# Kernel optimization log

Hardware: AMD Instinct MI355X
Metric: run time of the kernel (lower is better)

## Reference

```python
import math
import jax, jax.numpy as jnp
import numpy as np

B, S, D = 2, 2048, 1024
H, DK = 16, 64
NUM_BUCKETS = 32
MAX_DISTANCE = 128


def _relative_position_bucket(relative_position, num_buckets=NUM_BUCKETS, max_distance=MAX_DISTANCE):
    # bidirectional=True branch (encoder / non-causal)
    n = -relative_position
    num_buckets = num_buckets // 2
    ret = (n < 0).astype(jnp.int32) * num_buckets
    n = jnp.abs(n)
    max_exact = num_buckets // 2
    is_small = n < max_exact
    # guard log(0); masked out by is_small anyway
    n_safe = jnp.maximum(n, 1).astype(jnp.float32)
    val_if_large = max_exact + (
        jnp.log(n_safe / max_exact) / math.log(max_distance / max_exact) * (num_buckets - max_exact)
    ).astype(jnp.int32)
    val_if_large = jnp.minimum(val_if_large, num_buckets - 1)
    return ret + jnp.where(is_small, n, val_if_large)


def setup_inputs() -> dict:
    key = jax.random.key(0)
    ks = jax.random.split(key, 6)
    std_q = (D * DK) ** -0.5
    std = D ** -0.5
    return {
        "x": jax.random.normal(ks[0], (B, S, D), jnp.float32),
        "q_w": jax.random.normal(ks[1], (H * DK, D), jnp.float32) * std_q,
        "k_w": jax.random.normal(ks[2], (H * DK, D), jnp.float32) * std,
        "v_w": jax.random.normal(ks[3], (H * DK, D), jnp.float32) * std,
        "o_w": jax.random.normal(ks[4], (D, H * DK), jnp.float32) * ((H * DK) ** -0.5),
        "rel_bias": jax.random.normal(ks[5], (NUM_BUCKETS, H), jnp.float32) * std,
    }


def reference(x, q_w, k_w, v_w, o_w, rel_bias):
    b, s, _ = x.shape
    # project and split heads: [B, H, S, DK]
    def proj(w):
        return (x @ w.T).reshape(b, s, H, DK).transpose(0, 2, 1, 3)
    q, k, v = proj(q_w), proj(k_w), proj(v_w)

    # T5-style unscaled attention scores: [B, H, Sq, Sk]
    scores = jnp.einsum("bhqd,bhkd->bhqk", q, k)

    # bucketed relative-position bias
    ctx = jnp.arange(s)[:, None]
    mem = jnp.arange(s)[None, :]
    rp_bucket = _relative_position_bucket(mem - ctx)  # [S, S]
    bias = rel_bias[rp_bucket]                        # [S, S, H]
    bias = bias.transpose(2, 0, 1)[None]              # [1, H, S, S]
    scores = scores + bias

    attn = jax.nn.softmax(scores, axis=-1)
    ctx_out = jnp.einsum("bhqk,bhkd->bhqd", attn, v)
    ctx_out = ctx_out.transpose(0, 2, 1, 3).reshape(b, s, H * DK)
    return ctx_out @ o_w.T
```

## Files before the change

### kernel.cpp

```cpp
#include <hip/hip_runtime.h>
#include <stdint.h>


typedef unsigned short u16;
typedef __attribute__((ext_vector_type(8))) short short8;
typedef __attribute__((ext_vector_type(4))) float float4v;
typedef __attribute__((ext_vector_type(4))) u16 ushort4v;
typedef __attribute__((ext_vector_type(4))) uint32_t uint4v;

typedef __attribute__((address_space(1))) void void_g;
typedef __attribute__((address_space(3))) void void_l;

#define L2E 1.4426950408889634f

__device__ __forceinline__ u16 f2b(float f) {
  union { float f; uint32_t u; } v; v.f = f;
  uint32_t r = (v.u + 0x7fffu + ((v.u >> 16) & 1u)) >> 16;
  return (u16)r;
}
__device__ __forceinline__ u16 f2b_fast(float f) {
  union { float f; uint32_t u; } v; v.f = f;
  return (u16)((v.u + 0x8000u) >> 16);
}

__global__ void cvt_all(const float* __restrict__ x,  const float* __restrict__ qw,
                        const float* __restrict__ kw, const float* __restrict__ vw,
                        const float* __restrict__ ow, const float* __restrict__ rel_bias,
                        u16* __restrict__ xb, u16* __restrict__ wqkv, u16* __restrict__ owb,
                        float* __restrict__ biasT) {
  int bi = blockIdx.x;
  if (bi >= 8192) {
    int idx = (bi - 8192) * 256 + threadIdx.x;
    int h = idx >> 12, t = idx & 4095;
    if (t > 4094) { biasT[h * 4096 + 4095] = -1.0e4f; return; }
    int d = t - 2047;
    int n = -d;
    int ret = (n < 0) ? 16 : 0;
    int na = (n < 0) ? -n : n;
    int bucket;
    if (na < 8) {
      bucket = ret + na;
    } else {
      float v = logf((float)na / 8.0f) / logf(16.0f) * 8.0f;
      int vi = 8 + (int)v;
      bucket = ret + (vi > 15 ? 15 : vi);
    }
    biasT[h * 4096 + t] = (rel_bias[bucket * 16 + h] - 8.0f) * L2E;
    return;
  }
  int i = bi * 256 + threadIdx.x;
  const float* s; u16* d; int off;
  if (i < 1048576)      { s = x;  d = xb;              off = i; }
  else if (i < 1310720) { s = qw; d = wqkv;            off = i - 1048576; }
  else if (i < 1572864) { s = kw; d = wqkv + 1048576;  off = i - 1310720; }
  else if (i < 1835008) { s = vw; d = wqkv + 2097152;  off = i - 1572864; }
  else                  { s = ow; d = owb;             off = i - 1835008; }
  float4v v = ((const float4v*)s)[off];
  ushort4v o;
  o.x = f2b(v.x); o.y = f2b(v.y); o.z = f2b(v.z); o.w = f2b(v.w);
  ((ushort4v*)d)[off] = o;
}

__global__ __launch_bounds__(256, 2)
void gemm_qkv(const u16* __restrict__ A, const u16* __restrict__ W,
              u16* __restrict__ qkb, u16* __restrict__ vTp) {
  const int K = 1024;
  __shared__ __align__(16) char SM[34816];
  u16* As = (u16*)SM;
  u16* Bs = (u16*)(SM + 16384);
  const int tid = threadIdx.x;
  const int wid = tid >> 6;
  const int lane = tid & 63;
  const int row16 = lane & 15, oct = lane >> 4;
  const int tm = blockIdx.x * 128, tn = blockIdx.y * 128;
  const int wm = (wid & 1) * 64, wn = (wid >> 1) * 64;
  const int srow = lane >> 2;
  const int sc = (lane & 3) * 8;
  float4v acc[4][4] = {};
  for (int k0 = 0; k0 < K; k0 += 64) {
    __syncthreads();
#pragma unroll
    for (int i = 0; i < 4; i++) {
      const int idx = i * 4 + wid;
      const int kk = idx & 1;
      const int rb = idx >> 1;
      const int r = rb * 16 + srow;
      const int c = kk * 32 + sc;
      __builtin_amdgcn_global_load_lds((void_g*)(A + (size_t)(tm + r) * K + k0 + c),
                                       (void_l*)(As + (kk * 128 + rb * 16) * 32), 16, 0, 0);
      __builtin_amdgcn_global_load_lds((void_g*)(W + (size_t)(tn + r) * K + k0 + c),
                                       (void_l*)(Bs + (kk * 128 + rb * 16) * 32), 16, 0, 0);
    }
    __syncthreads();
#pragma unroll
    for (int kk = 0; kk < 2; kk++) {
      short8 af[4], bfr[4];
#pragma unroll
      for (int mi = 0; mi < 4; mi++)
        af[mi] = *(const short8*)(As + (kk * 128 + wm + mi * 16 + row16) * 32 + oct * 8);
#pragma unroll
      for (int ni = 0; ni < 4; ni++)
        bfr[ni] = *(const short8*)(Bs + (kk * 128 + wn + ni * 16 + row16) * 32 + oct * 8);
#pragma unroll
      for (int mi = 0; mi < 4; mi++)
#pragma unroll
        for (int ni = 0; ni < 4; ni++)
          acc[mi][ni] = __builtin_amdgcn_mfma_f32_16x16x32_bf16(af[mi], bfr[ni], acc[mi][ni], 0, 0, 0);
    }
  }

  u16* Es = (u16*)SM;
  __syncthreads();
#pragma unroll
  for (int mi = 0; mi < 4; mi++)
#pragma unroll
    for (int ni = 0; ni < 4; ni++)
#pragma unroll
      for (int r = 0; r < 4; r++)
        Es[(wm + mi * 16 + oct * 4 + r) * 136 + wn + ni * 16 + row16] = f2b(acc[mi][ni][r]);
  __syncthreads();

  if (tn < 2048) {
#pragma unroll
    for (int it = 0; it < 8; it++) {
      int idx = it * 256 + tid;
      int row = idx >> 4, c = idx & 15;
      short8 v = *(const short8*)(Es + row * 136 + c * 8);
      *(short8*)(qkb + (size_t)(tm + row) * 2048 + tn + c * 8) = v;
    }
  } else {
    const int h0 = (tn - 2048) >> 6;
    const int b = tm >> 11;
    const int s0 = tm & 2047;
#pragma unroll
    for (int it = 0; it < 8; it++) {
      int idx = it * 256 + tid;
      int dg = idx >> 4;
      int ch = idx & 15;
      short8 o;
#pragma unroll
      for (int j = 0; j < 8; j++) {
        int sp = ch * 8 + j;
        int sl = (sp & ~31) + (((sp >> 2) & 1) << 4) + (((sp >> 3) & 3) << 2) + (sp & 3);
        o[j] = (short)Es[sl * 136 + dg];
      }
      const int head = h0 + (dg >> 6), d = dg & 63;
      *(short8*)(vTp + ((size_t)((b * 16 + head) * 64 + d)) * 2048 + s0 + ch * 8) = o;
    }
  }
}

__global__ __launch_bounds__(256, 2)
void gemm_out(const u16* __restrict__ A, const u16* __restrict__ W,
              float* __restrict__ C) {
  const int K = 1024, N = 1024;
  __shared__ __align__(16) char SM[34816];
  u16* As = (u16*)SM;
  u16* Bs = (u16*)(SM + 8192);
  const int tid = threadIdx.x;
  const int wid = tid >> 6;
  const int lane = tid & 63;
  const int row16 = lane & 15, oct = lane >> 4;
  const int tm = blockIdx.x * 64, tn = blockIdx.y * 128;
  const int wm = (wid & 1) * 32, wn = (wid >> 1) * 64;
  const int srow = lane >> 2;
  const int sc = (lane & 3) * 8;
  float4v acc[2][4] = {};
  for (int k0 = 0; k0 < K; k0 += 64) {
    __syncthreads();
#pragma unroll
    for (int i = 0; i < 2; i++) {
      const int idx = i * 4 + wid;
      const int kk = idx & 1;
      const int rb = idx >> 1;
      const int r = rb * 16 + srow;
      const int c = kk * 32 + sc;
      __builtin_amdgcn_global_load_lds((void_g*)(A + (size_t)(tm + r) * K + k0 + c),
                                       (void_l*)(As + (kk * 64 + rb * 16) * 32), 16, 0, 0);
    }
#pragma unroll
    for (int i = 0; i < 4; i++) {
      const int idx = i * 4 + wid;
      const int kk = idx & 1;
      const int rb = idx >> 1;
      const int r = rb * 16 + srow;
      const int c = kk * 32 + sc;
      __builtin_amdgcn_global_load_lds((void_g*)(W + (size_t)(tn + r) * K + k0 + c),
                                       (void_l*)(Bs + (kk * 128 + rb * 16) * 32), 16, 0, 0);
    }
    __syncthreads();
#pragma unroll
    for (int kk = 0; kk < 2; kk++) {
      short8 af[2], bfr[4];
#pragma unroll
      for (int mi = 0; mi < 2; mi++)
        af[mi] = *(const short8*)(As + (kk * 64 + wm + mi * 16 + row16) * 32 + oct * 8);
#pragma unroll
      for (int ni = 0; ni < 4; ni++)
        bfr[ni] = *(const short8*)(Bs + (kk * 128 + wn + ni * 16 + row16) * 32 + oct * 8);
#pragma unroll
      for (int mi = 0; mi < 2; mi++)
#pragma unroll
        for (int ni = 0; ni < 4; ni++)
          acc[mi][ni] = __builtin_amdgcn_mfma_f32_16x16x32_bf16(af[mi], bfr[ni], acc[mi][ni], 0, 0, 0);
    }
  }
  float* Ef = (float*)SM;
  __syncthreads();
#pragma unroll
  for (int mi = 0; mi < 2; mi++)
#pragma unroll
    for (int ni = 0; ni < 4; ni++)
#pragma unroll
      for (int r = 0; r < 4; r++)
        Ef[(wm + mi * 16 + oct * 4 + r) * 132 + wn + ni * 16 + row16] = acc[mi][ni][r];
  __syncthreads();
#pragma unroll
  for (int it = 0; it < 8; it++) {
    int idx = it * 256 + tid;
    int row = idx >> 5, c = idx & 31;
    float4v v = *(const float4v*)(Ef + row * 132 + c * 4);
    *(float4v*)(C + (size_t)(tm + row) * N + tn + c * 4) = v;
  }
}

__global__ __launch_bounds__(256, 2)
void flash_attn(const u16* __restrict__ qkb, const u16* __restrict__ vTp,
                const float* __restrict__ biasT, u16* __restrict__ ctx) {
  const int S = 2048, LDQ = 2048;
  const int lin = blockIdx.x + (blockIdx.y << 4) + (blockIdx.z << 8);
  const int V = (lin & 7) * 64 + (lin >> 3);
  const int qt0 = (V & 15) * 128;
  const int h = (V >> 4) & 15, b = V >> 8;
  const int tid = threadIdx.x, wid = tid >> 6, lane = tid & 63;
  const int row16 = lane & 15, oct = lane >> 4;

  __shared__ __align__(16) float biasS[2176];
  __shared__ __align__(16) u16 Ks[2][64][40];
  __shared__ __align__(16) u16 Vts[2][64][40];

  {
    const float* bsrc = biasT + h * 4096 + (1920 - qt0);
    for (int i = tid; i < 544; i += 256)
      ((float4v*)biasS)[i] = ((const float4v*)bsrc)[i];
  }
  const float bias_neg = biasT[h * 4096];
  const float bias_pos = biasT[h * 4096 + 4094];

  const u16* qbase = qkb + ((size_t)b * S + qt0 + wid * 32) * LDQ + h * 64;
  short8 qf[2][2];
#pragma unroll
  for (int f = 0; f < 2; f++)
#pragma unroll
    for (int hd = 0; hd < 2; hd++)
      qf[f][hd] = *(const short8*)(qbase + (size_t)(f * 16 + row16) * LDQ + hd * 32 + oct * 8);

  float4v l_acc[2] = {};
  float4v o_acc[2][4] = {};
  const short8 ones = {0x3F80, 0x3F80, 0x3F80, 0x3F80, 0x3F80, 0x3F80, 0x3F80, 0x3F80};

  const int sr = lane >> 2, c8 = (lane & 3) * 8;
  const int srow = wid * 16 + sr;
  const u16* Kst = qkb + 1024 + ((size_t)b * S + srow) * LDQ + c8 + h * 64;
  const u16* Vst = vTp + ((size_t)(b * 16 + h) * 64 + srow) * 2048 + c8;

  short8 kreg[2], vreg[2];
#pragma unroll
  for (int hd = 0; hd < 2; hd++) kreg[hd] = *(const short8*)(Kst + hd * 32);
#pragma unroll
  for (int ks = 0; ks < 2; ks++) vreg[ks] = *(const short8*)(Vst + ks * 32);

  for (int kt = 0; kt < S; kt += 64) {
    __syncthreads();
#pragma unroll
    for (int hd = 0; hd < 2; hd++) *(short8*)&Ks[hd][srow][c8] = kreg[hd];
#pragma unroll
    for (int ks = 0; ks < 2; ks++) *(short8*)&Vts[ks][srow][c8] = vreg[ks];
    __syncthreads();

    if (kt + 64 < S) {
#pragma unroll
      for (int hd = 0; hd < 2; hd++)
        kreg[hd] = *(const short8*)(Kst + (size_t)(kt + 64) * LDQ + hd * 32);
#pragma unroll
      for (int ks = 0; ks < 2; ks++)
        vreg[ks] = *(const short8*)(Vst + (kt + 64) + ks * 32);
    }

    short8 kf[4][2];
#pragma unroll
    for (int st = 0; st < 4; st++)
#pragma unroll
      for (int hd = 0; hd < 2; hd++)
        kf[st][hd] = *(const short8*)&Ks[hd][st * 16 + row16][oct * 8];

    float4v sc[2][4];
    __builtin_amdgcn_s_setprio(1);
#pragma unroll
    for (int f = 0; f < 2; f++)
#pragma unroll
      for (int st = 0; st < 4; st++) {
        float4v s = {};
        s = __builtin_amdgcn_mfma_f32_16x16x32_bf16(kf[st][0], qf[f][0], s, 0, 0, 0);
        s = __builtin_amdgcn_mfma_f32_16x16x32_bf16(kf[st][1], qf[f][1], s, 0, 0, 0);
        sc[f][st] = s;
      }
    __builtin_amdgcn_s_setprio(0);

    short8 vf[2][4];
#pragma unroll
    for (int ks = 0; ks < 2; ks++)
#pragma unroll
      for (int ni = 0; ni < 4; ni++)
        vf[ks][ni] = *(const short8*)&Vts[ks][ni * 16 + row16][oct * 8];

    const int dk = kt - qt0;
    const bool far = (dk >= 256) || (dk <= -192);
    if (far) {
      const float bc = (dk > 0) ? bias_pos : bias_neg;
#pragma unroll
      for (int f = 0; f < 2; f++)
#pragma unroll
        for (int st = 0; st < 4; st++)
#pragma unroll
          for (int r = 0; r < 4; r++)
            sc[f][st][r] = __builtin_amdgcn_exp2f(__builtin_fmaf(sc[f][st][r], L2E, bc));
    } else {
#pragma unroll
      for (int f = 0; f < 2; f++) {
        const int basef = kt + oct * 4 - wid * 32 - f * 16 - row16 + 127;
#pragma unroll
        for (int st = 0; st < 4; st++)
#pragma unroll
          for (int r = 0; r < 4; r++)
            sc[f][st][r] = __builtin_amdgcn_exp2f(
                __builtin_fmaf(sc[f][st][r], L2E, biasS[basef + st * 16 + r]));
      }
    }

#pragma unroll
    for (int f = 0; f < 2; f++) {
#pragma unroll
      for (int ks = 0; ks < 2; ks++) {
        uint4v pw;
        pw.x = (uint32_t)f2b_fast(sc[f][2 * ks][0]) | ((uint32_t)f2b_fast(sc[f][2 * ks][1]) << 16);
        pw.y = (uint32_t)f2b_fast(sc[f][2 * ks][2]) | ((uint32_t)f2b_fast(sc[f][2 * ks][3]) << 16);
        pw.z = (uint32_t)f2b_fast(sc[f][2 * ks + 1][0]) | ((uint32_t)f2b_fast(sc[f][2 * ks + 1][1]) << 16);
        pw.w = (uint32_t)f2b_fast(sc[f][2 * ks + 1][2]) | ((uint32_t)f2b_fast(sc[f][2 * ks + 1][3]) << 16);
        short8 pf = __builtin_bit_cast(short8, pw);
        __builtin_amdgcn_s_setprio(1);
#pragma unroll
        for (int ni = 0; ni < 4; ni++)
          o_acc[f][ni] = __builtin_amdgcn_mfma_f32_16x16x32_bf16(pf, vf[ks][ni], o_acc[f][ni], 0, 0, 0);
        l_acc[f] = __builtin_amdgcn_mfma_f32_16x16x32_bf16(pf, ones, l_acc[f], 0, 0, 0);
        __builtin_amdgcn_s_setprio(0);
      }
    }
  }

#pragma unroll
  for (int f = 0; f < 2; f++) {
    float linv[4];
#pragma unroll
    for (int r = 0; r < 4; r++)
      linv[r] = 1.0f / l_acc[f][r];
    const size_t orow = (size_t)b * S + qt0 + wid * 32 + f * 16 + oct * 4;
#pragma unroll
    for (int ni = 0; ni < 4; ni++)
#pragma unroll
      for (int r = 0; r < 4; r++)
        ctx[(orow + r) * 1024 + h * 64 + ni * 16 + row16] = f2b_fast(o_acc[f][ni][r] * linv[r]);
  }
}

extern "C" void kernel_launch(void* const* d_in, const int* in_sizes, int n_in,
                              void* d_out, int out_size, void* d_ws, size_t ws_size,
                              hipStream_t stream) {
  const float* x        = (const float*)d_in[0];
  const float* q_w      = (const float*)d_in[1];
  const float* k_w      = (const float*)d_in[2];
  const float* v_w      = (const float*)d_in[3];
  const float* o_w      = (const float*)d_in[4];
  const float* rel_bias = (const float*)d_in[5];

  char* ws = (char*)d_ws;
  u16*   xb    = (u16*)(ws);
  u16*   wqkv  = (u16*)(ws + 8388608);
  u16*   owb   = (u16*)(ws + 14680064);
  u16*   qkb   = (u16*)(ws + 16777216);
  u16*   vTp   = (u16*)(ws + 33554432);
  u16*   ctxb  = (u16*)(ws + 41943040);
  float* biasT = (float*)(ws + 50331648);

  cvt_all<<<8448, 256, 0, stream>>>(x, q_w, k_w, v_w, o_w, rel_bias,
                                    xb, wqkv, owb, biasT);

  dim3 g1(4096 / 128, 3072 / 128);
  gemm_qkv<<<g1, 256, 0, stream>>>(xb, wqkv, qkb, vTp);

  dim3 g2(2048 / 128, 16, 2);
  flash_attn<<<g2, 256, 0, stream>>>(qkb, vTp, biasT, ctxb);

  dim3 g3(4096 / 64, 1024 / 128);
  gemm_out<<<g3, 256, 0, stream>>>(ctxb, owb, (float*)d_out);
}
```

Before: 181.3 us.

## Halve flash-attention query tile to 64 rows and raise occupancy to 4 blocks

The attention kernel's query tile shrinks from 128 to 64 rows per block, so each wave handles 16 query rows instead of 32. The grid doubles, launch bounds ask for 4 blocks per CU, and the shared bias window is cut to a fixed 384-entry slice around the diagonal. The goal is more resident waves and more blocks to fill the GPU, trading away K/V reuse: every K/V tile is now loaded from global and staged through shared memory twice as often per query row.

```diff
diff --git a/kernel.cpp b/kernel.cpp
--- a/kernel.cpp
+++ b/kernel.cpp
@@ -224,39 +224,36 @@
   }
 }
 
-__global__ __launch_bounds__(256, 2)
+__global__ __launch_bounds__(256, 4)
 void flash_attn(const u16* __restrict__ qkb, const u16* __restrict__ vTp,
                 const float* __restrict__ biasT, u16* __restrict__ ctx) {
   const int S = 2048, LDQ = 2048;
-  const int lin = blockIdx.x + (blockIdx.y << 4) + (blockIdx.z << 8);
-  const int V = (lin & 7) * 64 + (lin >> 3);
-  const int qt0 = (V & 15) * 128;
-  const int h = (V >> 4) & 15, b = V >> 8;
+  const int lin = blockIdx.x + (blockIdx.y << 5) + (blockIdx.z << 9);
+  const int V = (lin & 7) * 128 + (lin >> 3);
+  const int qt0 = (V & 31) * 64;
+  const int h = (V >> 5) & 15, b = V >> 9;
   const int tid = threadIdx.x, wid = tid >> 6, lane = tid & 63;
   const int row16 = lane & 15, oct = lane >> 4;
 
-  __shared__ __align__(16) float biasS[2176];
+  __shared__ __align__(16) float biasS[384];
   __shared__ __align__(16) u16 Ks[2][64][40];
   __shared__ __align__(16) u16 Vts[2][64][40];
 
   {
-    const float* bsrc = biasT + h * 4096 + (1920 - qt0);
-    for (int i = tid; i < 544; i += 256)
-      ((float4v*)biasS)[i] = ((const float4v*)bsrc)[i];
+    const float* bsrc = biasT + h * 4096 + 1856;
+    if (tid < 96) ((float4v*)biasS)[tid] = ((const float4v*)bsrc)[tid];
   }
   const float bias_neg = biasT[h * 4096];
   const float bias_pos = biasT[h * 4096 + 4094];
 
-  const u16* qbase = qkb + ((size_t)b * S + qt0 + wid * 32) * LDQ + h * 64;
-  short8 qf[2][2];
-#pragma unroll
-  for (int f = 0; f < 2; f++)
-#pragma unroll
-    for (int hd = 0; hd < 2; hd++)
-      qf[f][hd] = *(const short8*)(qbase + (size_t)(f * 16 + row16) * LDQ + hd * 32 + oct * 8);
-
-  float4v l_acc[2] = {};
-  float4v o_acc[2][4] = {};
+  const u16* qbase = qkb + ((size_t)b * S + qt0 + wid * 16) * LDQ + h * 64;
+  short8 qf[2];
+#pragma unroll
+  for (int hd = 0; hd < 2; hd++)
+    qf[hd] = *(const short8*)(qbase + (size_t)row16 * LDQ + hd * 32 + oct * 8);
+
+  float4v l_acc = {};
+  float4v o_acc[4] = {};
   const short8 ones = {0x3F80, 0x3F80, 0x3F80, 0x3F80, 0x3F80, 0x3F80, 0x3F80, 0x3F80};
 
   const int sr = lane >> 2, c8 = (lane & 3) * 8;
@@ -294,17 +291,15 @@
       for (int hd = 0; hd < 2; hd++)
         kf[st][hd] = *(const short8*)&Ks[hd][st * 16 + row16][oct * 8];
 
-    float4v sc[2][4];
+    float4v sc[4];
     __builtin_amdgcn_s_setprio(1);
 #pragma unroll
-    for (int f = 0; f < 2; f++)
-#pragma unroll
-      for (int st = 0; st < 4; st++) {
-        float4v s = {};
-        s = __builtin_amdgcn_mfma_f32_16x16x32_bf16(kf[st][0], qf[f][0], s, 0, 0, 0);
-        s = __builtin_amdgcn_mfma_f32_16x16x32_bf16(kf[st][1], qf[f][1], s, 0, 0, 0);
-        sc[f][st] = s;
-      }
+    for (int st = 0; st < 4; st++) {
+      float4v s = {};
+      s = __builtin_amdgcn_mfma_f32_16x16x32_bf16(kf[st][0], qf[0], s, 0, 0, 0);
+      s = __builtin_amdgcn_mfma_f32_16x16x32_bf16(kf[st][1], qf[1], s, 0, 0, 0);
+      sc[st] = s;
+    }
     __builtin_amdgcn_s_setprio(0);
 
     short8 vf[2][4];
@@ -315,62 +310,51 @@
         vf[ks][ni] = *(const short8*)&Vts[ks][ni * 16 + row16][oct * 8];
 
     const int dk = kt - qt0;
-    const bool far = (dk >= 256) || (dk <= -192);
+    const bool far = (dk >= 192) || (dk <= -192);
     if (far) {
       const float bc = (dk > 0) ? bias_pos : bias_neg;
 #pragma unroll
-      for (int f = 0; f < 2; f++)
-#pragma unroll
-        for (int st = 0; st < 4; st++)
-#pragma unroll
-          for (int r = 0; r < 4; r++)
-            sc[f][st][r] = __builtin_amdgcn_exp2f(__builtin_fmaf(sc[f][st][r], L2E, bc));
+      for (int st = 0; st < 4; st++)
+#pragma unroll
+        for (int r = 0; r < 4; r++)
+          sc[st][r] = __builtin_amdgcn_exp2f(__builtin_fmaf(sc[st][r], L2E, bc));
     } else {
-#pragma unroll
-      for (int f = 0; f < 2; f++) {
-        const int basef = kt + oct * 4 - wid * 32 - f * 16 - row16 + 127;
-#pragma unroll
-        for (int st = 0; st < 4; st++)
-#pragma unroll
-          for (int r = 0; r < 4; r++)
-            sc[f][st][r] = __builtin_amdgcn_exp2f(
-                __builtin_fmaf(sc[f][st][r], L2E, biasS[basef + st * 16 + r]));
-      }
-    }
-
-#pragma unroll
-    for (int f = 0; f < 2; f++) {
-#pragma unroll
-      for (int ks = 0; ks < 2; ks++) {
-        uint4v pw;
-        pw.x = (uint32_t)f2b_fast(sc[f][2 * ks][0]) | ((uint32_t)f2b_fast(sc[f][2 * ks][1]) << 16);
-        pw.y = (uint32_t)f2b_fast(sc[f][2 * ks][2]) | ((uint32_t)f2b_fast(sc[f][2 * ks][3]) << 16);
-        pw.z = (uint32_t)f2b_fast(sc[f][2 * ks + 1][0]) | ((uint32_t)f2b_fast(sc[f][2 * ks + 1][1]) << 16);
-        pw.w = (uint32_t)f2b_fast(sc[f][2 * ks + 1][2]) | ((uint32_t)f2b_fast(sc[f][2 * ks + 1][3]) << 16);
-        short8 pf = __builtin_bit_cast(short8, pw);
-        __builtin_amdgcn_s_setprio(1);
-#pragma unroll
-        for (int ni = 0; ni < 4; ni++)
-          o_acc[f][ni] = __builtin_amdgcn_mfma_f32_16x16x32_bf16(pf, vf[ks][ni], o_acc[f][ni], 0, 0, 0);
-        l_acc[f] = __builtin_amdgcn_mfma_f32_16x16x32_bf16(pf, ones, l_acc[f], 0, 0, 0);
-        __builtin_amdgcn_s_setprio(0);
-      }
-    }
-  }
-
-#pragma unroll
-  for (int f = 0; f < 2; f++) {
-    float linv[4];
+      const int basef = dk + oct * 4 - wid * 16 - row16 + 191;
+#pragma unroll
+      for (int st = 0; st < 4; st++)
+#pragma unroll
+        for (int r = 0; r < 4; r++)
+          sc[st][r] = __builtin_amdgcn_exp2f(
+              __builtin_fmaf(sc[st][r], L2E, biasS[basef + st * 16 + r]));
+    }
+
+#pragma unroll
+    for (int ks = 0; ks < 2; ks++) {
+      uint4v pw;
+      pw.x = (uint32_t)f2b_fast(sc[2 * ks][0]) | ((uint32_t)f2b_fast(sc[2 * ks][1]) << 16);
+      pw.y = (uint32_t)f2b_fast(sc[2 * ks][2]) | ((uint32_t)f2b_fast(sc[2 * ks][3]) << 16);
+      pw.z = (uint32_t)f2b_fast(sc[2 * ks + 1][0]) | ((uint32_t)f2b_fast(sc[2 * ks + 1][1]) << 16);
+      pw.w = (uint32_t)f2b_fast(sc[2 * ks + 1][2]) | ((uint32_t)f2b_fast(sc[2 * ks + 1][3]) << 16);
+      short8 pf = __builtin_bit_cast(short8, pw);
+      __builtin_amdgcn_s_setprio(1);
+#pragma unroll
+      for (int ni = 0; ni < 4; ni++)
+        o_acc[ni] = __builtin_amdgcn_mfma_f32_16x16x32_bf16(pf, vf[ks][ni], o_acc[ni], 0, 0, 0);
+      l_acc = __builtin_amdgcn_mfma_f32_16x16x32_bf16(pf, ones, l_acc, 0, 0, 0);
+      __builtin_amdgcn_s_setprio(0);
+    }
+  }
+
+  float linv[4];
+#pragma unroll
+  for (int r = 0; r < 4; r++)
+    linv[r] = 1.0f / l_acc[r];
+  const size_t orow = (size_t)b * S + qt0 + wid * 16 + oct * 4;
+#pragma unroll
+  for (int ni = 0; ni < 4; ni++)
 #pragma unroll
     for (int r = 0; r < 4; r++)
-      linv[r] = 1.0f / l_acc[f][r];
-    const size_t orow = (size_t)b * S + qt0 + wid * 32 + f * 16 + oct * 4;
-#pragma unroll
-    for (int ni = 0; ni < 4; ni++)
-#pragma unroll
-      for (int r = 0; r < 4; r++)
-        ctx[(orow + r) * 1024 + h * 64 + ni * 16 + row16] = f2b_fast(o_acc[f][ni][r] * linv[r]);
-  }
+      ctx[(orow + r) * 1024 + h * 64 + ni * 16 + row16] = f2b_fast(o_acc[ni][r] * linv[r]);
 }
 
 extern "C" void kernel_launch(void* const* d_in, const int* in_sizes, int n_in,
@@ -398,7 +382,7 @@
   dim3 g1(4096 / 128, 3072 / 128);
   gemm_qkv<<<g1, 256, 0, stream>>>(xb, wqkv, qkb, vTp);
 
-  dim3 g2(2048 / 128, 16, 2);
+  dim3 g2(2048 / 64, 16, 2);
   flash_attn<<<g2, 256, 0, stream>>>(qkb, vTp, biasT, ctxb);
 
   dim3 g3(4096 / 64, 1024 / 128);
```

Result: slower. 191.6 us (+5.7%).

## Double-buffer LDS tiles in projection GEMMs and swizzle QKV block order

Applied to the files above, without the earlier changes.

Both the QKV and output-projection GEMMs now use two LDS stages. The next K-slice's global_load_lds is issued before the MFMA work on the current slice, and only one barrier per iteration remains, so global-load latency can overlap compute. The QKV kernel also remaps the linear block index into a permuted tile order, meant to improve L2 reuse of shared A/W rows. The cost is more LDS per block (64KB for QKV, 48KB for the output GEMM), which could limit occupancy.

```diff
diff --git a/kernel.cpp b/kernel.cpp
--- a/kernel.cpp
+++ b/kernel.cpp
@@ -65,33 +65,44 @@
 void gemm_qkv(const u16* __restrict__ A, const u16* __restrict__ W,
               u16* __restrict__ qkb, u16* __restrict__ vTp) {
   const int K = 1024;
-  __shared__ __align__(16) char SM[34816];
-  u16* As = (u16*)SM;
-  u16* Bs = (u16*)(SM + 16384);
+  __shared__ __align__(16) char SM[65536];
   const int tid = threadIdx.x;
   const int wid = tid >> 6;
   const int lane = tid & 63;
   const int row16 = lane & 15, oct = lane >> 4;
-  const int tm = blockIdx.x * 128, tn = blockIdx.y * 128;
+  const int lin = blockIdx.x + blockIdx.y * 32;
+  const int V = (lin & 7) * 96 + (lin >> 3);
+  const int bx = V & 31, by = V >> 5;
+  const int tm = bx * 128, tn = by * 128;
   const int wm = (wid & 1) * 64, wn = (wid >> 1) * 64;
   const int srow = lane >> 2;
   const int sc = (lane & 3) * 8;
   float4v acc[4][4] = {};
-  for (int k0 = 0; k0 < K; k0 += 64) {
-    __syncthreads();
-#pragma unroll
-    for (int i = 0; i < 4; i++) {
-      const int idx = i * 4 + wid;
-      const int kk = idx & 1;
-      const int rb = idx >> 1;
-      const int r = rb * 16 + srow;
-      const int c = kk * 32 + sc;
-      __builtin_amdgcn_global_load_lds((void_g*)(A + (size_t)(tm + r) * K + k0 + c),
-                                       (void_l*)(As + (kk * 128 + rb * 16) * 32), 16, 0, 0);
-      __builtin_amdgcn_global_load_lds((void_g*)(W + (size_t)(tn + r) * K + k0 + c),
-                                       (void_l*)(Bs + (kk * 128 + rb * 16) * 32), 16, 0, 0);
-    }
-    __syncthreads();
+
+#define STAGE_QKV(buf, k0)                                                            \
+  {                                                                                   \
+    u16* Ad = (u16*)(SM + (buf) * 32768);                                             \
+    u16* Bd = (u16*)(SM + (buf) * 32768 + 16384);                                     \
+    _Pragma("unroll")                                                                 \
+    for (int i = 0; i < 4; i++) {                                                     \
+      const int idx = i * 4 + wid;                                                    \
+      const int kk = idx & 1;                                                         \
+      const int rb = idx >> 1;                                                        \
+      const int r = rb * 16 + srow;                                                   \
+      const int c = kk * 32 + sc;                                                     \
+      __builtin_amdgcn_global_load_lds((void_g*)(A + (size_t)(tm + r) * K + (k0) + c),\
+                                       (void_l*)(Ad + (kk * 128 + rb * 16) * 32), 16, 0, 0); \
+      __builtin_amdgcn_global_load_lds((void_g*)(W + (size_t)(tn + r) * K + (k0) + c),\
+                                       (void_l*)(Bd + (kk * 128 + rb * 16) * 32), 16, 0, 0); \
+    }                                                                                 \
+  }
+
+  STAGE_QKV(0, 0);
+  __syncthreads();
+  for (int t = 0; t < 16; t++) {
+    if (t + 1 < 16) STAGE_QKV((t + 1) & 1, (t + 1) * 64);
+    const u16* As = (const u16*)(SM + (t & 1) * 32768);
+    const u16* Bs = As + 8192;
 #pragma unroll
     for (int kk = 0; kk < 2; kk++) {
       short8 af[4], bfr[4];
@@ -107,10 +118,10 @@
         for (int ni = 0; ni < 4; ni++)
           acc[mi][ni] = __builtin_amdgcn_mfma_f32_16x16x32_bf16(af[mi], bfr[ni], acc[mi][ni], 0, 0, 0);
     }
+    __syncthreads();
   }
 
   u16* Es = (u16*)SM;
-  __syncthreads();
 #pragma unroll
   for (int mi = 0; mi < 4; mi++)
 #pragma unroll
@@ -154,9 +165,7 @@
 void gemm_out(const u16* __restrict__ A, const u16* __restrict__ W,
               float* __restrict__ C) {
   const int K = 1024, N = 1024;
-  __shared__ __align__(16) char SM[34816];
-  u16* As = (u16*)SM;
-  u16* Bs = (u16*)(SM + 8192);
+  __shared__ __align__(16) char SM[49152];
   const int tid = threadIdx.x;
   const int wid = tid >> 6;
   const int lane = tid & 63;
@@ -166,29 +175,39 @@
   const int srow = lane >> 2;
   const int sc = (lane & 3) * 8;
   float4v acc[2][4] = {};
-  for (int k0 = 0; k0 < K; k0 += 64) {
-    __syncthreads();
-#pragma unroll
-    for (int i = 0; i < 2; i++) {
-      const int idx = i * 4 + wid;
-      const int kk = idx & 1;
-      const int rb = idx >> 1;
-      const int r = rb * 16 + srow;
-      const int c = kk * 32 + sc;
-      __builtin_amdgcn_global_load_lds((void_g*)(A + (size_t)(tm + r) * K + k0 + c),
-                                       (void_l*)(As + (kk * 64 + rb * 16) * 32), 16, 0, 0);
-    }
-#pragma unroll
-    for (int i = 0; i < 4; i++) {
-      const int idx = i * 4 + wid;
-      const int kk = idx & 1;
-      const int rb = idx >> 1;
-      const int r = rb * 16 + srow;
-      const int c = kk * 32 + sc;
-      __builtin_amdgcn_global_load_lds((void_g*)(W + (size_t)(tn + r) * K + k0 + c),
-                                       (void_l*)(Bs + (kk * 128 + rb * 16) * 32), 16, 0, 0);
-    }
-    __syncthreads();
+
+#define STAGE_OUT(buf, k0)                                                            \
+  {                                                                                   \
+    u16* Ad = (u16*)(SM + (buf) * 24576);                                             \
+    u16* Bd = (u16*)(SM + (buf) * 24576 + 8192);                                      \
+    _Pragma("unroll")                                                                 \
+    for (int i = 0; i < 2; i++) {                                                     \
+      const int idx = i * 4 + wid;                                                    \
+      const int kk = idx & 1;                                                         \
+      const int rb = idx >> 1;                                                        \
+      const int r = rb * 16 + srow;                                                   \
+      const int c = kk * 32 + sc;                                                     \
+      __builtin_amdgcn_global_load_lds((void_g*)(A + (size_t)(tm + r) * K + (k0) + c),\
+                                       (void_l*)(Ad + (kk * 64 + rb * 16) * 32), 16, 0, 0); \
+    }                                                                                 \
+    _Pragma("unroll")                                                                 \
+    for (int i = 0; i < 4; i++) {                                                     \
+      const int idx = i * 4 + wid;                                                    \
+      const int kk = idx & 1;                                                         \
+      const int rb = idx >> 1;                                                        \
+      const int r = rb * 16 + srow;                                                   \
+      const int c = kk * 32 + sc;                                                     \
+      __builtin_amdgcn_global_load_lds((void_g*)(W + (size_t)(tn + r) * K + (k0) + c),\
+                                       (void_l*)(Bd + (kk * 128 + rb * 16) * 32), 16, 0, 0); \
+    }                                                                                 \
+  }
+
+  STAGE_OUT(0, 0);
+  __syncthreads();
+  for (int t = 0; t < 16; t++) {
+    if (t + 1 < 16) STAGE_OUT((t + 1) & 1, (t + 1) * 64);
+    const u16* As = (const u16*)(SM + (t & 1) * 24576);
+    const u16* Bs = As + 4096;
 #pragma unroll
     for (int kk = 0; kk < 2; kk++) {
       short8 af[2], bfr[4];
@@ -204,9 +223,9 @@
         for (int ni = 0; ni < 4; ni++)
           acc[mi][ni] = __builtin_amdgcn_mfma_f32_16x16x32_bf16(af[mi], bfr[ni], acc[mi][ni], 0, 0, 0);
     }
+    __syncthreads();
   }
   float* Ef = (float*)SM;
-  __syncthreads();
 #pragma unroll
   for (int mi = 0; mi < 2; mi++)
 #pragma unroll
```

Measured after the change: 179.2 us. Within noise of the previous version (-1.1%).
